# Kernel optimization log

Hardware: AMD Instinct MI355X
Metric: run time of the kernel (lower is better)

Reference implementation:

```python
import jax, jax.numpy as jnp
import numpy as np

B, T, M, F, H, O = 64, 168, 256, 32, 128, 32
TWO_OVER_PI = 2.0 / np.pi


def setup_inputs() -> dict:
    key = jax.random.key(0)
    ks = jax.random.split(key, 8)
    return {
        "x": jax.random.normal(ks[0], (B, T, M, F), dtype=jnp.float32),
        "assoc_W": jax.random.normal(ks[1], (F, M, M), dtype=jnp.float32) * (1.0 / np.sqrt(M)),
        "W_ih": jax.random.normal(ks[2], (4 * H, F), dtype=jnp.float32) * (1.0 / np.sqrt(F)),
        "W_hh": jax.random.normal(ks[3], (4 * H, H), dtype=jnp.float32) * (1.0 / np.sqrt(H)),
        "b_ih": jax.random.normal(ks[4], (4 * H,), dtype=jnp.float32) * 0.01,
        "b_hh": jax.random.normal(ks[5], (4 * H,), dtype=jnp.float32) * 0.01,
        "dense_W": jax.random.normal(ks[6], (O, H), dtype=jnp.float32) * (1.0 / np.sqrt(H)),
        "dense_b": jax.random.normal(ks[7], (O,), dtype=jnp.float32) * 0.01,
    }


def _forward(x, assoc_W, W_ih, W_hh, b_ih, b_hh, dense_W, dense_b):
    # x: [B, T, M, F] (batch_first) -> scan over time
    xt = jnp.transpose(x, (1, 0, 2, 3))  # [T, B, M, F]
    b, m = x.shape[0], x.shape[2]
    h0 = jnp.zeros((b, m, H), dtype=x.dtype)
    c0 = jnp.zeros((b, m, H), dtype=x.dtype)

    def step(carry, xin):
        h, c = carry
        # ArcTanNorm: squash into (-1, 1)
        y = jnp.arctan(xin) * TWO_OVER_PI                      # [B, M, F]
        # ICFA: per-attribute association across map units
        y = jnp.einsum('amn,bna->bma', assoc_W, y)             # [B, M, F]
        # LSTM cell (shared weights across map units), PyTorch gate order i,f,g,o
        gates = (jnp.einsum('bmf,gf->bmg', y, W_ih) + b_ih
                 + jnp.einsum('bmh,gh->bmg', h, W_hh) + b_hh)  # [B, M, 4H]
        i, f, g, o = jnp.split(gates, 4, axis=-1)
        i, f, o = jax.nn.sigmoid(i), jax.nn.sigmoid(f), jax.nn.sigmoid(o)
        g = jnp.tanh(g)
        c = f * c + i * g
        h = o * jnp.tanh(c)
        # Dense output head
        out = jnp.einsum('bmh,oh->bmo', h, dense_W) + dense_b  # [B, M, O]
        return (h, c), out

    _, outs = jax.lax.scan(step, (h0, c0), xt)                 # [T, B, M, O]
    return jnp.transpose(outs, (1, 0, 2, 3))                   # [B, T, M, O]


def reference(x, assoc_W, W_ih, W_hh, b_ih, b_hh, dense_W, dense_b):
    return _forward(x, assoc_W, W_ih, W_hh, b_ih, b_hh, dense_W, dense_b)
```

## Files before the change

### kernel.cpp

```cpp
#include <hip/hip_runtime.h>

#define B_  64
#define T_  168
#define M_  256
#define F_  32
#define H_  128
#define O_  32
#define BT_ (B_*T_)

typedef __attribute__((ext_vector_type(8))) short bh8;
typedef __attribute__((ext_vector_type(4))) short sh4;
typedef __attribute__((ext_vector_type(4))) float fx4;

static __device__ __forceinline__ short f2bf(float f) {
  unsigned u = __float_as_uint(f);
  u += 0x7FFFu + ((u >> 16) & 1u);
  return (short)(u >> 16);
}
static __device__ __forceinline__ unsigned cvtpk(float lo, float hi) {
  unsigned r;
  asm("v_cvt_pk_bf16_f32 %0, %1, %2" : "=v"(r) : "v"(lo), "v"(hi));
  return r;
}
static __device__ __forceinline__ float ex2_(float x) {
#if __has_builtin(__builtin_amdgcn_exp2f)
  return __builtin_amdgcn_exp2f(x);
#else
  return exp2f(x);
#endif
}
static __device__ __forceinline__ float rcp_(float x) {
#if __has_builtin(__builtin_amdgcn_rcpf)
  return __builtin_amdgcn_rcpf(x);
#else
  return 1.0f / x;
#endif
}
static __device__ __forceinline__ float sigm(float x) {
  return 1.0f / (1.0f + __expf(-x));
}
static __device__ __forceinline__ float tanh_f(float x) {
  return 1.0f - 2.0f / (1.0f + __expf(2.0f * x));
}
static __device__ __forceinline__ fx4 mm16(bh8 a, bh8 b, fx4 c) {
  return __builtin_amdgcn_mfma_f32_16x16x32_bf16(a, b, c, 0, 0, 0);
}
static __device__ __forceinline__ bh8 cvt8(fx4 p0, fx4 p1) {
  bh8 s;
  s[0] = f2bf(p0[0]); s[1] = f2bf(p0[1]); s[2] = f2bf(p0[2]); s[3] = f2bf(p0[3]);
  s[4] = f2bf(p1[0]); s[5] = f2bf(p1[1]); s[6] = f2bf(p1[2]); s[7] = f2bf(p1[3]);
  return s;
}


__global__ __launch_bounds__(512) void atan_tr(const float* __restrict__ x,
                                               short* __restrict__ ut) {
  __shared__ __align__(16) short tl[8 * 32 * 68];
  const int tid = threadIdx.x;
  const float c2p = 0.63661977236758134f;
  for (int it = 0; it < 21; ++it) {
    const int id = blockIdx.x + it * 256;
    const int bt0 = (id >> 2) * 8, n0 = (id & 3) * 64;
    if (it) __syncthreads();
#pragma unroll
    for (int i = 0; i < 8; ++i) {
      int idx = tid + i * 512;
      int aq = idx & 7, nl = (idx >> 3) & 63, btl = idx >> 9;
      const float* src = x + (long)(bt0 + btl) * 8192 + (n0 + nl) * 32 + aq * 4;
      fx4 v = *(const fx4*)src;
      int base = (btl * 32 + aq * 4) * 68 + nl;
#pragma unroll
      for (int k = 0; k < 4; ++k)
        tl[base + k * 68] = f2bf(atanf(v[k]) * c2p);
    }
    __syncthreads();
#pragma unroll
    for (int p = 0; p < 8; ++p) {
      int r = p * 32 + (tid >> 4);
      int a = r >> 3, btl = r & 7, nq = tid & 15;
      sh4 v = *(const sh4*)&tl[(btl * 32 + a) * 68 + nq * 4];
      *(sh4*)&ut[((long)a * BT_ + bt0 + btl) * 256 + n0 + nq * 4] = v;
    }
  }
}

__global__ __launch_bounds__(512) void icfa_gemm(const short* __restrict__ ut,
                                                 const float* __restrict__ aw,
                                                 short* __restrict__ y) {
  __shared__ __align__(16) short waf[8 * 8 * 64 * 8];
  __shared__ __align__(16) short ubf[64 * 256];
  const int tid = threadIdx.x;
  const int lane = tid & 63, w = tid >> 6, l15 = lane & 15, l4 = lane >> 4;
  const int a = blockIdx.x >> 3, s = blockIdx.x & 7;
  const long ua = (long)a * BT_;

  for (int mh = 0; mh < 2; ++mh) {
    __syncthreads();
    for (int i = 0; i < 8; ++i) {
      int idx = tid + i * 512;
      int ln = idx & 63, ks = (idx >> 6) & 7, mt = idx >> 9;
      const float* src = aw + a * 65536 + (mh * 128 + mt * 16 + (ln & 15)) * 256
                         + ks * 32 + (ln >> 4) * 8;
      *(bh8*)&waf[idx * 8] = cvt8(*(const fx4*)src, *(const fx4*)(src + 4));
    }
    __syncthreads();
    bh8 Af[8];
#pragma unroll
    for (int ks = 0; ks < 8; ++ks)
      Af[ks] = *(const bh8*)&waf[((w * 8 + ks) * 64 + lane) * 8];

    for (int tile = 0; tile < 21; ++tile) {
      const int bt0 = s * 1344 + tile * 64;
      __syncthreads();
#pragma unroll
      for (int i = 0; i < 4; ++i) {
        int idx = tid + i * 512;
        int row = idx >> 5, slot = idx & 31;
        bh8 v = *(const bh8*)&ut[(ua + bt0 + row) * 256 + slot * 8];
        int sb = (row * 512 + slot * 16) ^ ((row & 7) << 4);
        *(bh8*)&((char*)ubf)[sb] = v;
      }
      __syncthreads();
#pragma unroll
      for (int ct = 0; ct < 4; ++ct) {
        fx4 acc = {0.f, 0.f, 0.f, 0.f};
        const int btr = ct * 16 + l15;
#pragma unroll
        for (int ks = 0; ks < 8; ++ks) {
          int byo = (btr * 512 + ks * 64 + l4 * 16) ^ ((btr & 7) << 4);
          bh8 Bf = *(const bh8*)&((char*)ubf)[byo];
          acc = mm16(Af[ks], Bf, acc);
        }
        sh4 o;
        o[0] = f2bf(acc[0]); o[1] = f2bf(acc[1]);
        o[2] = f2bf(acc[2]); o[3] = f2bf(acc[3]);
        *(sh4*)&y[(ua + bt0 + btr) * 256 + mh * 128 + w * 16 + l4 * 4] = o;
      }
    }
  }
}

__global__ __launch_bounds__(1024) void lstm_fused6(
    const short* __restrict__ y,
    const float* __restrict__ Wih, const float* __restrict__ Whh,
    const float* __restrict__ bih, const float* __restrict__ bhh,
    const float* __restrict__ dW,  const float* __restrict__ db,
    float* __restrict__ out) {
  __shared__ __align__(16) short whf[65536];
  __shared__ __align__(16) short hx[8704];
  __shared__ __align__(16) short ytr[2048];
  const int tid = threadIdx.x;
  const int lane = tid & 63, w = tid >> 6, l15 = lane & 15, l4 = lane >> 4;
  const int wg = w & 7, hw = w >> 3;
  const int bidx = blockIdx.x >> 2, m0 = (blockIdx.x & 3) * 64;
  const float L2E = 1.4426950408889634f;

  for (int i = 0; i < 8; ++i) {
    int idx = tid + i * 1024;
    int ln = idx & 63, ks = (idx >> 6) & 3, gate = (idx >> 8) & 3, wgp = idx >> 10;
    const float* src = Whh + ((gate * 8 + wgp) * 16 + (ln & 15)) * 128
                       + ks * 32 + (ln >> 4) * 8;
    *(bh8*)&whf[idx * 8] = cvt8(*(const fx4*)src, *(const fx4*)(src + 4));
  }
  for (int i = 0; i < 5; ++i) {
    int j = tid + i * 1024;
    if (j < 4352) ((int*)hx)[j] = 0;
  }

  bh8 wfih[4]; float nb[4][4];
#pragma unroll
  for (int gate = 0; gate < 4; ++gate) {
    int grow = (gate * 8 + wg) * 16;
    const float* src = Wih + (grow + l15) * 32 + l4 * 8;
    wfih[gate] = cvt8(*(const fx4*)src, *(const fx4*)(src + 4));
#pragma unroll
    for (int r = 0; r < 4; ++r) {
      int g = grow + l4 * 4 + r;
      float b = bih[g] + bhh[g];
      nb[gate][r] = (gate == 2) ? (2.0f * L2E * b) : (-L2E * b);
    }
  }
  bh8 df[4]; float dbv[4];
  const int oc = wg & 1, mt_d = hw * 2 + ((wg >> 1) & 1);
#pragma unroll
  for (int ks = 0; ks < 4; ++ks) {
    const float* src = dW + (oc * 16 + l15) * 128 + ks * 32 + l4 * 8;
    df[ks] = cvt8(*(const fx4*)src, *(const fx4*)(src + 4));
  }
#pragma unroll
  for (int r = 0; r < 4; ++r) dbv[r] = db[oc * 16 + l4 * 4 + r];

  float cst[2][4];
#pragma unroll
  for (int mt = 0; mt < 2; ++mt)
#pragma unroll
    for (int r = 0; r < 4; ++r) cst[mt][r] = 0.f;

  char* hxc = (char*)hx;
  const int hrb = (hw * 32 + l15) * 272 + l4 * 16;
  const int hdb = (mt_d * 16 + l15) * 272 + l4 * 16;
  const int hwb = (hw * 32 + l15) * 272 + wg * 32 + l4 * 8;
  const int ar = tid >> 5, mq2 = tid & 31;
  const long yrow = (long)ar * BT_ + (long)bidx * T_;
  const int ml0 = mq2 * 2;
  const int R0 = (ml0 >> 4) * 64 + ((ar >> 3) << 4) + (ml0 & 15);
  const int ytre0 = R0 * 8 + (ar & 7);
  const long obB = (long)bidx * T_ * 8192
                 + (long)(m0 + mt_d * 16 + l15) * 32 + oc * 16 + l4 * 4;

  int ys = *(const int*)&y[(yrow + 0) * 256 + m0 + mq2 * 2];
  ytr[ytre0]     = (short)(ys & 0xffff);
  ytr[ytre0 + 8] = (short)(((unsigned)ys) >> 16);
  ys = *(const int*)&y[(yrow + 1) * 256 + m0 + mq2 * 2];
  __syncthreads();

  for (int t = 0; t < T_; ++t) {
    int ysn = 0;
    if (t + 2 < T_) ysn = *(const int*)&y[(yrow + t + 2) * 256 + m0 + mq2 * 2];
    fx4 acc[4][2];
    {
      bh8 yB0 = *(const bh8*)&ytr[((2 * hw) * 64 + lane) * 8];
      bh8 yB1 = *(const bh8*)&ytr[((2 * hw + 1) * 64 + lane) * 8];
      fx4 Z = {0.f, 0.f, 0.f, 0.f};
#pragma unroll
      for (int g = 0; g < 4; ++g) {
        acc[g][0] = mm16(wfih[g], yB0, Z);
        acc[g][1] = mm16(wfih[g], yB1, Z);
      }
    }
#pragma unroll
    for (int ks = 0; ks < 4; ++ks) {
      bh8 hB0 = *(const bh8*)(hxc + hrb + ks * 64);
      bh8 hB1 = *(const bh8*)(hxc + hrb + 4352 + ks * 64);
#pragma unroll
      for (int g = 0; g < 4; ++g) {
        bh8 Af = *(const bh8*)((const char*)whf
                               + ((wg * 16 + g * 4 + ks) * 64 + lane) * 16);
        acc[g][0] = mm16(Af, hB0, acc[g][0]);
        acc[g][1] = mm16(Af, hB1, acc[g][1]);
      }
    }
    if (wg < 4 && t > 0) {
      fx4 A = {dbv[0], dbv[1], dbv[2], dbv[3]};
#pragma unroll
      for (int ks = 0; ks < 4; ++ks) {
        bh8 hd = *(const bh8*)(hxc + hdb + ks * 64);
        A = mm16(df[ks], hd, A);
      }
      *(fx4*)&out[obB + (long)(t - 1) * 8192] = A;
    }
    float hn[2][4];
#pragma unroll
    for (int mt = 0; mt < 2; ++mt)
#pragma unroll
      for (int r = 0; r < 4; ++r) {
        float iv = rcp_(1.f + ex2_(fmaf(acc[0][mt][r], -L2E, nb[0][r])));
        float fv = rcp_(1.f + ex2_(fmaf(acc[1][mt][r], -L2E, nb[1][r])));
        float ov = rcp_(1.f + ex2_(fmaf(acc[3][mt][r], -L2E, nb[3][r])));
        float gv = 1.f - 2.f * rcp_(1.f + ex2_(fmaf(acc[2][mt][r], 2.f * L2E, nb[2][r])));
        float cn = fv * cst[mt][r] + iv * gv;
        cst[mt][r] = cn;
        float th = 1.f - 2.f * rcp_(1.f + ex2_(cn * (2.f * L2E)));
        hn[mt][r] = ov * th;
      }
    __syncthreads();
#pragma unroll
    for (int mt = 0; mt < 2; ++mt) {
      unsigned p01 = cvtpk(hn[mt][0], hn[mt][1]);
      unsigned p23 = cvtpk(hn[mt][2], hn[mt][3]);
      *(unsigned long long*)(hxc + hwb + mt * 4352) =
          (((unsigned long long)p23) << 32) | p01;
    }
    if (t + 1 < T_) {
      ytr[ytre0]     = (short)(ys & 0xffff);
      ytr[ytre0 + 8] = (short)(((unsigned)ys) >> 16);
    }
    ys = ysn;
    __syncthreads();
  }
  if (wg < 4) {
    fx4 A = {dbv[0], dbv[1], dbv[2], dbv[3]};
#pragma unroll
    for (int ks = 0; ks < 4; ++ks) {
      bh8 hd = *(const bh8*)(hxc + hdb + ks * 64);
      A = mm16(df[ks], hd, A);
    }
    *(fx4*)&out[obB + (long)(T_ - 1) * 8192] = A;
  }
}


__global__ __launch_bounds__(512) void icfa_mfma(const float* __restrict__ x,
                                                 const float* __restrict__ aw,
                                                 float* __restrict__ y) {
  __shared__ short waf[8 * 8 * 64 * 8];
  __shared__ short ubf[64 * 264];
  const int tid = threadIdx.x;
  const int lane = tid & 63, w = tid >> 6, l15 = lane & 15, l4 = lane >> 4;
  const int a = blockIdx.x >> 3, s = blockIdx.x & 7;
  const float c2p = 0.63661977236758134f;

  for (int mh = 0; mh < 2; ++mh) {
    __syncthreads();
    for (int i = 0; i < 8; ++i) {
      int idx = tid + i * 512;
      int ln = idx & 63, ks = (idx >> 6) & 7, mt = idx >> 9;
      const float* src = aw + a * 65536 + (mh * 128 + mt * 16 + (ln & 15)) * 256
                         + ks * 32 + (ln >> 4) * 8;
      *(bh8*)&waf[idx * 8] = cvt8(*(const fx4*)src, *(const fx4*)(src + 4));
    }
    __syncthreads();
    bh8 Af[8];
#pragma unroll
    for (int ks = 0; ks < 8; ++ks)
      Af[ks] = *(const bh8*)&waf[((w * 8 + ks) * 64 + lane) * 8];

    for (int tile = 0; tile < 21; ++tile) {
      const int bt0 = s * 1344 + tile * 64;
      __syncthreads();
#pragma unroll 4
      for (int i = 0; i < 32; ++i) {
        int idx = tid + i * 512;
        int n = idx & 255, btc = idx >> 8;
        float v = x[(long)(bt0 + btc) * 8192 + n * 32 + a];
        ubf[btc * 264 + n] = f2bf(atanf(v) * c2p);
      }
      __syncthreads();
#pragma unroll
      for (int ct = 0; ct < 4; ++ct) {
        fx4 acc = {0.f, 0.f, 0.f, 0.f};
#pragma unroll
        for (int ks = 0; ks < 8; ++ks) {
          bh8 Bf = *(const bh8*)&ubf[(ct * 16 + l15) * 264 + ks * 32 + l4 * 8];
          acc = mm16(Af[ks], Bf, acc);
        }
        long ybase = (long)(bt0 + ct * 16 + l15) * 8192
                     + (mh * 128 + w * 16 + l4 * 4) * 32 + a;
#pragma unroll
        for (int r = 0; r < 4; ++r) y[ybase + (long)r * 32] = acc[r];
      }
    }
  }
}

__global__ __launch_bounds__(512) void lstm_fused(
    const float* __restrict__ Wih, const float* __restrict__ Whh,
    const float* __restrict__ bih, const float* __restrict__ bhh,
    const float* __restrict__ dW,  const float* __restrict__ db,
    float* __restrict__ yo) {
  __shared__ short whf[32 * 4 * 64 * 8];
  __shared__ short hbuf[4 * 4 * 64 * 8];
  __shared__ short ytr[4 * 64 * 8];
  __shared__ float obuf[64 * 36];
  const int tid = threadIdx.x;
  const int lane = tid & 63, w = tid >> 6, l15 = lane & 15, l4 = lane >> 4;
  const int bidx = blockIdx.x >> 2, m0 = (blockIdx.x & 3) * 64;

  for (int i = 0; i < 16; ++i) {
    int idx = tid + i * 512;
    int ln = idx & 63, ks = (idx >> 6) & 3, ct = idx >> 8;
    const float* src = Whh + (ct * 16 + (ln & 15)) * 128 + ks * 32 + (ln >> 4) * 8;
    *(bh8*)&whf[idx * 8] = cvt8(*(const fx4*)src, *(const fx4*)(src + 4));
  }
  for (int i = 0; i < 8; ++i) ((int*)hbuf)[tid + i * 512] = 0;

  bh8 wfih[4]; float bias[4];
#pragma unroll
  for (int gate = 0; gate < 4; ++gate) {
    int g = (gate * 8 + w) * 16 + l15;
    bias[gate] = bih[g] + bhh[g];
    const float* src = Wih + g * 32 + l4 * 8;
    wfih[gate] = cvt8(*(const fx4*)src, *(const fx4*)(src + 4));
  }
  bh8 df[4];
  const int rtd = w >> 1, oc = w & 1;
  const int od = oc * 16 + l15;
  const float dbias = db[od];
#pragma unroll
  for (int ks = 0; ks < 4; ++ks) {
    const float* src = dW + od * 128 + ks * 32 + l4 * 8;
    df[ks] = cvt8(*(const fx4*)src, *(const fx4*)(src + 4));
  }

  float cst[4][4];
#pragma unroll
  for (int rt = 0; rt < 4; ++rt)
#pragma unroll
    for (int r = 0; r < 4; ++r) cst[rt][r] = 0.f;

  const int mloc = tid >> 3, a0 = (tid & 7) * 4;
  const long tb0 = (long)bidx * T_ * 8192;
  const long pfoff = (long)(m0 + mloc) * 32 + a0;
  const int ytre = ((mloc >> 4) * 64 + ((a0 >> 3) << 4) + (mloc & 15)) * 8 + (a0 & 7);
  const int kse = w >> 1;
  const int lnhi = (((w & 1) * 2 + (l15 >> 3)) << 4);
  const int e0 = l15 & 7;

  fx4 y4 = *(const fx4*)&yo[tb0 + pfoff];
  {
    sh4 p; p[0] = f2bf(y4[0]); p[1] = f2bf(y4[1]); p[2] = f2bf(y4[2]); p[3] = f2bf(y4[3]);
    *(sh4*)&ytr[ytre] = p;
  }
  y4 = *(const fx4*)&yo[tb0 + 8192 + pfoff];
  __syncthreads();

  for (int t = 0; t < T_; ++t) {
    const long off = tb0 + (long)t * 8192;
    float hn[4][4];
    bh8 Ball[4][4];
#pragma unroll
    for (int gate = 0; gate < 4; ++gate)
#pragma unroll
      for (int ks = 0; ks < 4; ++ks)
        Ball[gate][ks] =
            *(const bh8*)&whf[((((gate * 8 + w) * 4) + ks) * 64 + lane) * 8];
#pragma unroll
    for (int rt = 0; rt < 4; ++rt) {
      bh8 ya = *(const bh8*)&ytr[(rt * 64 + lane) * 8];
      bh8 hA[4];
#pragma unroll
      for (int ks = 0; ks < 4; ++ks)
        hA[ks] = *(const bh8*)&hbuf[((rt * 4 + ks) * 64 + lane) * 8];
      fx4 acc[4];
#pragma unroll
      for (int gate = 0; gate < 4; ++gate) {
        fx4 A = {bias[gate], bias[gate], bias[gate], bias[gate]};
        A = mm16(ya, wfih[gate], A);
#pragma unroll
        for (int ks = 0; ks < 4; ++ks) A = mm16(hA[ks], Ball[gate][ks], A);
        acc[gate] = A;
      }
#pragma unroll
      for (int r = 0; r < 4; ++r) {
        float iv = sigm(acc[0][r]);
        float fv = sigm(acc[1][r]);
        float gv = tanh_f(acc[2][r]);
        float ov = sigm(acc[3][r]);
        float cn = fv * cst[rt][r] + iv * gv;
        cst[rt][r] = cn;
        hn[rt][r] = ov * tanh_f(cn);
      }
    }
    __syncthreads();
#pragma unroll
    for (int rt = 0; rt < 4; ++rt)
#pragma unroll
      for (int r = 0; r < 4; ++r)
        hbuf[((rt * 4 + kse) * 64 + lnhi + l4 * 4 + r) * 8 + e0] = f2bf(hn[rt][r]);
    if (t + 1 < T_) {
      sh4 p; p[0] = f2bf(y4[0]); p[1] = f2bf(y4[1]); p[2] = f2bf(y4[2]); p[3] = f2bf(y4[3]);
      *(sh4*)&ytr[ytre] = p;
    }
    if (t + 2 < T_) y4 = *(const fx4*)&yo[off + 2 * 8192 + pfoff];
    __syncthreads();
    {
      fx4 A = {dbias, dbias, dbias, dbias};
#pragma unroll
      for (int ks = 0; ks < 4; ++ks) {
        bh8 hA2 = *(const bh8*)&hbuf[((rtd * 4 + ks) * 64 + lane) * 8];
        A = mm16(hA2, df[ks], A);
      }
#pragma unroll
      for (int r = 0; r < 4; ++r)
        obuf[(rtd * 16 + l4 * 4 + r) * 36 + oc * 16 + l15] = A[r];
    }
    __syncthreads();
    {
      fx4 o4 = *(const fx4*)&obuf[mloc * 36 + a0];
      *(fx4*)&yo[off + pfoff] = o4;
    }
  }
}

extern "C" void kernel_launch(void* const* d_in, const int* in_sizes, int n_in,
                              void* d_out, int out_size, void* d_ws, size_t ws_size,
                              hipStream_t stream) {
  const float* x   = (const float*)d_in[0];
  const float* aw  = (const float*)d_in[1];
  const float* wih = (const float*)d_in[2];
  const float* whh = (const float*)d_in[3];
  const float* bih = (const float*)d_in[4];
  const float* bhh = (const float*)d_in[5];
  const float* dw  = (const float*)d_in[6];
  const float* db  = (const float*)d_in[7];
  float* out = (float*)d_out;

  const size_t PLANE = (size_t)32 * BT_ * 256;
  const size_t NEED  = 2 * PLANE * sizeof(short);
  if (d_ws && ws_size >= NEED) {
    short* u = (short*)d_ws;
    short* yv = u + PLANE;
    hipLaunchKernelGGL(atan_tr,   dim3(256), dim3(512), 0, stream, x, u);
    hipLaunchKernelGGL(icfa_gemm, dim3(256), dim3(512), 0, stream, u, aw, yv);
    hipLaunchKernelGGL(lstm_fused6, dim3(256), dim3(1024), 0, stream,
                       yv, wih, whh, bih, bhh, dw, db, out);
  } else {
    hipLaunchKernelGGL(icfa_mfma, dim3(256), dim3(512), 0, stream, x, aw, out);
    hipLaunchKernelGGL(lstm_fused, dim3(256), dim3(512), 0, stream,
                       wih, whh, bih, bhh, dw, db, out);
  }
}
```

Baseline: 854.6 us.

## Double-buffer LSTM h/y LDS tiles, keep input-gate weights in registers, fuse gate math

Double-buffers the hidden-state and input tiles in shared memory, so each timestep needs one barrier instead of two; new h is written to the alternate buffer. The input-gate W_hh fragment now lives in registers, which frees LDS and cuts per-step LDS reads. The sigmoid/tanh gate math is rewritten algebraically to share reciprocals, giving fewer rcp instructions. Costs are more registers and LDS for the doubled buffers, plus a possible small numerical change from the combined reciprocals.

```diff
diff --git a/kernel.cpp b/kernel.cpp
--- a/kernel.cpp
+++ b/kernel.cpp
@@ -140,31 +140,37 @@
   }
 }
 
-__global__ __launch_bounds__(1024) void lstm_fused6(
+__global__ __launch_bounds__(1024) void lstm_fused7(
     const short* __restrict__ y,
     const float* __restrict__ Wih, const float* __restrict__ Whh,
     const float* __restrict__ bih, const float* __restrict__ bhh,
     const float* __restrict__ dW,  const float* __restrict__ db,
     float* __restrict__ out) {
-  __shared__ __align__(16) short whf[65536];
-  __shared__ __align__(16) short hx[8704];
-  __shared__ __align__(16) short ytr[2048];
+  __shared__ __align__(16) short whf[49152];
+  __shared__ __align__(16) short hx[17408];
+  __shared__ __align__(16) short ytr[4096];
   const int tid = threadIdx.x;
   const int lane = tid & 63, w = tid >> 6, l15 = lane & 15, l4 = lane >> 4;
   const int wg = w & 7, hw = w >> 3;
   const int bidx = blockIdx.x >> 2, m0 = (blockIdx.x & 3) * 64;
   const float L2E = 1.4426950408889634f;
 
-  for (int i = 0; i < 8; ++i) {
+  for (int i = 0; i < 6; ++i) {
     int idx = tid + i * 1024;
-    int ln = idx & 63, ks = (idx >> 6) & 3, gate = (idx >> 8) & 3, wgp = idx >> 10;
-    const float* src = Whh + ((gate * 8 + wgp) * 16 + (ln & 15)) * 128
+    int ln = idx & 63, ks = (idx >> 6) & 3, wgp = (idx >> 8) & 7, gm1 = idx >> 11;
+    const float* src = Whh + (((gm1 + 1) * 8 + wgp) * 16 + (ln & 15)) * 128
                        + ks * 32 + (ln >> 4) * 8;
     *(bh8*)&whf[idx * 8] = cvt8(*(const fx4*)src, *(const fx4*)(src + 4));
   }
-  for (int i = 0; i < 5; ++i) {
+  for (int i = 0; i < 9; ++i) {
     int j = tid + i * 1024;
-    if (j < 4352) ((int*)hx)[j] = 0;
+    if (j < 8704) ((int*)hx)[j] = 0;
+  }
+  bh8 wrg[4];
+#pragma unroll
+  for (int ks = 0; ks < 4; ++ks) {
+    const float* src = Whh + (wg * 16 + l15) * 128 + ks * 32 + l4 * 8;
+    wrg[ks] = cvt8(*(const fx4*)src, *(const fx4*)(src + 4));
   }
 
   bh8 wfih[4]; float nb[4][4];
@@ -214,13 +220,14 @@
   ys = *(const int*)&y[(yrow + 1) * 256 + m0 + mq2 * 2];
   __syncthreads();
 
+  int pbo = 0, pbi = 0;
   for (int t = 0; t < T_; ++t) {
     int ysn = 0;
     if (t + 2 < T_) ysn = *(const int*)&y[(yrow + t + 2) * 256 + m0 + mq2 * 2];
     fx4 acc[4][2];
     {
-      bh8 yB0 = *(const bh8*)&ytr[((2 * hw) * 64 + lane) * 8];
-      bh8 yB1 = *(const bh8*)&ytr[((2 * hw + 1) * 64 + lane) * 8];
+      bh8 yB0 = *(const bh8*)&ytr[pbi + ((2 * hw) * 64 + lane) * 8];
+      bh8 yB1 = *(const bh8*)&ytr[pbi + ((2 * hw + 1) * 64 + lane) * 8];
       fx4 Z = {0.f, 0.f, 0.f, 0.f};
 #pragma unroll
       for (int g = 0; g < 4; ++g) {
@@ -230,12 +237,14 @@
     }
 #pragma unroll
     for (int ks = 0; ks < 4; ++ks) {
-      bh8 hB0 = *(const bh8*)(hxc + hrb + ks * 64);
-      bh8 hB1 = *(const bh8*)(hxc + hrb + 4352 + ks * 64);
-#pragma unroll
-      for (int g = 0; g < 4; ++g) {
+      bh8 hB0 = *(const bh8*)(hxc + pbo + hrb + ks * 64);
+      bh8 hB1 = *(const bh8*)(hxc + pbo + hrb + 4352 + ks * 64);
+      acc[0][0] = mm16(wrg[ks], hB0, acc[0][0]);
+      acc[0][1] = mm16(wrg[ks], hB1, acc[0][1]);
+#pragma unroll
+      for (int g = 1; g < 4; ++g) {
         bh8 Af = *(const bh8*)((const char*)whf
-                               + ((wg * 16 + g * 4 + ks) * 64 + lane) * 16);
+                               + (g - 1) * 32768 + wg * 4096 + ks * 1024 + lane * 16);
         acc[g][0] = mm16(Af, hB0, acc[g][0]);
         acc[g][1] = mm16(Af, hB1, acc[g][1]);
       }
@@ -244,7 +253,7 @@
       fx4 A = {dbv[0], dbv[1], dbv[2], dbv[3]};
 #pragma unroll
       for (int ks = 0; ks < 4; ++ks) {
-        bh8 hd = *(const bh8*)(hxc + hdb + ks * 64);
+        bh8 hd = *(const bh8*)(hxc + pbo + hdb + ks * 64);
         A = mm16(df[ks], hd, A);
       }
       *(fx4*)&out[obB + (long)(t - 1) * 8192] = A;
@@ -254,35 +263,38 @@
     for (int mt = 0; mt < 2; ++mt)
 #pragma unroll
       for (int r = 0; r < 4; ++r) {
-        float iv = rcp_(1.f + ex2_(fmaf(acc[0][mt][r], -L2E, nb[0][r])));
-        float fv = rcp_(1.f + ex2_(fmaf(acc[1][mt][r], -L2E, nb[1][r])));
-        float ov = rcp_(1.f + ex2_(fmaf(acc[3][mt][r], -L2E, nb[3][r])));
-        float gv = 1.f - 2.f * rcp_(1.f + ex2_(fmaf(acc[2][mt][r], 2.f * L2E, nb[2][r])));
-        float cn = fv * cst[mt][r] + iv * gv;
+        float eI = ex2_(fmaf(acc[0][mt][r], -L2E, nb[0][r]));
+        float eF = ex2_(fmaf(acc[1][mt][r], -L2E, nb[1][r]));
+        float eG = ex2_(fmaf(acc[2][mt][r], 2.f * L2E, nb[2][r]));
+        float eO = ex2_(fmaf(acc[3][mt][r], -L2E, nb[3][r]));
+        float pi = 1.f + eI, pf = 1.f + eF, pg = 1.f + eG;
+        float pig = pi * pg;
+        float num = fmaf(cst[mt][r], pig, (eG - 1.f) * pf);
+        float cn = num * rcp_(pf * pig);
         cst[mt][r] = cn;
-        float th = 1.f - 2.f * rcp_(1.f + ex2_(cn * (2.f * L2E)));
-        hn[mt][r] = ov * th;
-      }
-    __syncthreads();
+        float eC = ex2_(cn * (2.f * L2E));
+        hn[mt][r] = (eC - 1.f) * rcp_((1.f + eO) * (1.f + eC));
+      }
 #pragma unroll
     for (int mt = 0; mt < 2; ++mt) {
       unsigned p01 = cvtpk(hn[mt][0], hn[mt][1]);
       unsigned p23 = cvtpk(hn[mt][2], hn[mt][3]);
-      *(unsigned long long*)(hxc + hwb + mt * 4352) =
+      *(unsigned long long*)(hxc + (pbo ^ 17408) + hwb + mt * 4352) =
           (((unsigned long long)p23) << 32) | p01;
     }
     if (t + 1 < T_) {
-      ytr[ytre0]     = (short)(ys & 0xffff);
-      ytr[ytre0 + 8] = (short)(((unsigned)ys) >> 16);
+      ytr[(pbi ^ 2048) + ytre0]     = (short)(ys & 0xffff);
+      ytr[(pbi ^ 2048) + ytre0 + 8] = (short)(((unsigned)ys) >> 16);
     }
     ys = ysn;
     __syncthreads();
+    pbo ^= 17408; pbi ^= 2048;
   }
   if (wg < 4) {
     fx4 A = {dbv[0], dbv[1], dbv[2], dbv[3]};
 #pragma unroll
     for (int ks = 0; ks < 4; ++ks) {
-      bh8 hd = *(const bh8*)(hxc + hdb + ks * 64);
+      bh8 hd = *(const bh8*)(hxc + pbo + hdb + ks * 64);
       A = mm16(df[ks], hd, A);
     }
     *(fx4*)&out[obB + (long)(T_ - 1) * 8192] = A;
@@ -492,7 +504,7 @@
     short* yv = u + PLANE;
     hipLaunchKernelGGL(atan_tr,   dim3(256), dim3(512), 0, stream, x, u);
     hipLaunchKernelGGL(icfa_gemm, dim3(256), dim3(512), 0, stream, u, aw, yv);
-    hipLaunchKernelGGL(lstm_fused6, dim3(256), dim3(1024), 0, stream,
+    hipLaunchKernelGGL(lstm_fused7, dim3(256), dim3(1024), 0, stream,
                        yv, wih, whh, bih, bhh, dw, db, out);
   } else {
     hipLaunchKernelGGL(icfa_mfma, dim3(256), dim3(512), 0, stream, x, aw, out);
```

Result: slower. 933.3 us (+9.2%).

## Keep recurrent LSTM weights in registers and halve block size

Applied to the files above, without the earlier changes.

The LSTM kernel drops the 128KB shared-memory copy of W_hh and keeps each wave's W_hh fragments in registers. Blocks shrink from 1024 to 512 threads, with each wave covering all four 16-row m-tiles instead of two. The aim is to remove per-step LDS weight reads and the large LDS footprint, and to allow two blocks per CU under the new launch bounds. In exchange, register pressure rises (64 extra VGPRs of weights plus doubled accumulators and cell state), which risks spilling or lower occupancy. Fewer waves are also available to hide the serial per-timestep latency.

```diff
diff --git a/kernel.cpp b/kernel.cpp
--- a/kernel.cpp
+++ b/kernel.cpp
@@ -140,32 +140,31 @@
   }
 }
 
-__global__ __launch_bounds__(1024) void lstm_fused6(
+__global__ __launch_bounds__(512, 2) void lstm_fused8(
     const short* __restrict__ y,
     const float* __restrict__ Wih, const float* __restrict__ Whh,
     const float* __restrict__ bih, const float* __restrict__ bhh,
     const float* __restrict__ dW,  const float* __restrict__ db,
     float* __restrict__ out) {
-  __shared__ __align__(16) short whf[65536];
   __shared__ __align__(16) short hx[8704];
   __shared__ __align__(16) short ytr[2048];
   const int tid = threadIdx.x;
-  const int lane = tid & 63, w = tid >> 6, l15 = lane & 15, l4 = lane >> 4;
-  const int wg = w & 7, hw = w >> 3;
+  const int lane = tid & 63, wg = tid >> 6, l15 = lane & 15, l4 = lane >> 4;
   const int bidx = blockIdx.x >> 2, m0 = (blockIdx.x & 3) * 64;
   const float L2E = 1.4426950408889634f;
 
-  for (int i = 0; i < 8; ++i) {
-    int idx = tid + i * 1024;
-    int ln = idx & 63, ks = (idx >> 6) & 3, gate = (idx >> 8) & 3, wgp = idx >> 10;
-    const float* src = Whh + ((gate * 8 + wgp) * 16 + (ln & 15)) * 128
-                       + ks * 32 + (ln >> 4) * 8;
-    *(bh8*)&whf[idx * 8] = cvt8(*(const fx4*)src, *(const fx4*)(src + 4));
-  }
-  for (int i = 0; i < 5; ++i) {
-    int j = tid + i * 1024;
+  for (int i = 0; i < 9; ++i) {
+    int j = tid + i * 512;
     if (j < 4352) ((int*)hx)[j] = 0;
   }
+  bh8 wrg[4][4];
+#pragma unroll
+  for (int g = 0; g < 4; ++g)
+#pragma unroll
+    for (int ks = 0; ks < 4; ++ks) {
+      const float* src = Whh + ((g * 8 + wg) * 16 + l15) * 128 + ks * 32 + l4 * 8;
+      wrg[g][ks] = cvt8(*(const fx4*)src, *(const fx4*)(src + 4));
+    }
 
   bh8 wfih[4]; float nb[4][4];
 #pragma unroll
@@ -181,7 +180,7 @@
     }
   }
   bh8 df[4]; float dbv[4];
-  const int oc = wg & 1, mt_d = hw * 2 + ((wg >> 1) & 1);
+  const int oc = wg >> 2, mt_d = wg & 3;
 #pragma unroll
   for (int ks = 0; ks < 4; ++ks) {
     const float* src = dW + (oc * 16 + l15) * 128 + ks * 32 + l4 * 8;
@@ -190,57 +189,57 @@
 #pragma unroll
   for (int r = 0; r < 4; ++r) dbv[r] = db[oc * 16 + l4 * 4 + r];
 
-  float cst[2][4];
-#pragma unroll
-  for (int mt = 0; mt < 2; ++mt)
+  float cst[4][4];
+#pragma unroll
+  for (int mt = 0; mt < 4; ++mt)
 #pragma unroll
     for (int r = 0; r < 4; ++r) cst[mt][r] = 0.f;
 
   char* hxc = (char*)hx;
-  const int hrb = (hw * 32 + l15) * 272 + l4 * 16;
+  const int hrb = l15 * 272 + l4 * 16;
   const int hdb = (mt_d * 16 + l15) * 272 + l4 * 16;
-  const int hwb = (hw * 32 + l15) * 272 + wg * 32 + l4 * 8;
-  const int ar = tid >> 5, mq2 = tid & 31;
+  const int hwb = l15 * 272 + wg * 32 + l4 * 8;
+  const int ar = tid >> 4, mq = tid & 15;
   const long yrow = (long)ar * BT_ + (long)bidx * T_;
-  const int ml0 = mq2 * 2;
-  const int R0 = (ml0 >> 4) * 64 + ((ar >> 3) << 4) + (ml0 & 15);
-  const int ytre0 = R0 * 8 + (ar & 7);
+  const int ytre = ((mq >> 2) * 64 + ((ar >> 3) << 4) + (mq & 3) * 4) * 8 + (ar & 7);
   const long obB = (long)bidx * T_ * 8192
                  + (long)(m0 + mt_d * 16 + l15) * 32 + oc * 16 + l4 * 4;
 
-  int ys = *(const int*)&y[(yrow + 0) * 256 + m0 + mq2 * 2];
-  ytr[ytre0]     = (short)(ys & 0xffff);
-  ytr[ytre0 + 8] = (short)(((unsigned)ys) >> 16);
-  ys = *(const int*)&y[(yrow + 1) * 256 + m0 + mq2 * 2];
+  sh4 ys = *(const sh4*)&y[(yrow + 0) * 256 + m0 + mq * 4];
+#pragma unroll
+  for (int j = 0; j < 4; ++j) ytr[ytre + j * 8] = ys[j];
+  ys = *(const sh4*)&y[(yrow + 1) * 256 + m0 + mq * 4];
   __syncthreads();
 
   for (int t = 0; t < T_; ++t) {
-    int ysn = 0;
-    if (t + 2 < T_) ysn = *(const int*)&y[(yrow + t + 2) * 256 + m0 + mq2 * 2];
-    fx4 acc[4][2];
+    sh4 ysn = {0, 0, 0, 0};
+    if (t + 2 < T_) ysn = *(const sh4*)&y[(yrow + t + 2) * 256 + m0 + mq * 4];
+    fx4 acc[4][4];
     {
-      bh8 yB0 = *(const bh8*)&ytr[((2 * hw) * 64 + lane) * 8];
-      bh8 yB1 = *(const bh8*)&ytr[((2 * hw + 1) * 64 + lane) * 8];
+      bh8 yB[4];
+#pragma unroll
+      for (int mt = 0; mt < 4; ++mt)
+        yB[mt] = *(const bh8*)&ytr[(mt * 64 + lane) * 8];
       fx4 Z = {0.f, 0.f, 0.f, 0.f};
 #pragma unroll
-      for (int g = 0; g < 4; ++g) {
-        acc[g][0] = mm16(wfih[g], yB0, Z);
-        acc[g][1] = mm16(wfih[g], yB1, Z);
-      }
+      for (int g = 0; g < 4; ++g)
+#pragma unroll
+        for (int mt = 0; mt < 4; ++mt)
+          acc[g][mt] = mm16(wfih[g], yB[mt], Z);
     }
 #pragma unroll
     for (int ks = 0; ks < 4; ++ks) {
-      bh8 hB0 = *(const bh8*)(hxc + hrb + ks * 64);
-      bh8 hB1 = *(const bh8*)(hxc + hrb + 4352 + ks * 64);
-#pragma unroll
-      for (int g = 0; g < 4; ++g) {
-        bh8 Af = *(const bh8*)((const char*)whf
-                               + ((wg * 16 + g * 4 + ks) * 64 + lane) * 16);
-        acc[g][0] = mm16(Af, hB0, acc[g][0]);
-        acc[g][1] = mm16(Af, hB1, acc[g][1]);
-      }
-    }
-    if (wg < 4 && t > 0) {
+      bh8 hB[4];
+#pragma unroll
+      for (int mt = 0; mt < 4; ++mt)
+        hB[mt] = *(const bh8*)(hxc + hrb + mt * 4352 + ks * 64);
+#pragma unroll
+      for (int g = 0; g < 4; ++g)
+#pragma unroll
+        for (int mt = 0; mt < 4; ++mt)
+          acc[g][mt] = mm16(wrg[g][ks], hB[mt], acc[g][mt]);
+    }
+    if (t > 0) {
       fx4 A = {dbv[0], dbv[1], dbv[2], dbv[3]};
 #pragma unroll
       for (int ks = 0; ks < 4; ++ks) {
@@ -249,9 +248,9 @@
       }
       *(fx4*)&out[obB + (long)(t - 1) * 8192] = A;
     }
-    float hn[2][4];
-#pragma unroll
-    for (int mt = 0; mt < 2; ++mt)
+    float hn[4][4];
+#pragma unroll
+    for (int mt = 0; mt < 4; ++mt)
 #pragma unroll
       for (int r = 0; r < 4; ++r) {
         float iv = rcp_(1.f + ex2_(fmaf(acc[0][mt][r], -L2E, nb[0][r])));
@@ -265,20 +264,20 @@
       }
     __syncthreads();
 #pragma unroll
-    for (int mt = 0; mt < 2; ++mt) {
+    for (int mt = 0; mt < 4; ++mt) {
       unsigned p01 = cvtpk(hn[mt][0], hn[mt][1]);
       unsigned p23 = cvtpk(hn[mt][2], hn[mt][3]);
       *(unsigned long long*)(hxc + hwb + mt * 4352) =
           (((unsigned long long)p23) << 32) | p01;
     }
     if (t + 1 < T_) {
-      ytr[ytre0]     = (short)(ys & 0xffff);
-      ytr[ytre0 + 8] = (short)(((unsigned)ys) >> 16);
+#pragma unroll
+      for (int j = 0; j < 4; ++j) ytr[ytre + j * 8] = ys[j];
     }
     ys = ysn;
     __syncthreads();
   }
-  if (wg < 4) {
+  {
     fx4 A = {dbv[0], dbv[1], dbv[2], dbv[3]};
 #pragma unroll
     for (int ks = 0; ks < 4; ++ks) {
@@ -492,7 +491,7 @@
     short* yv = u + PLANE;
     hipLaunchKernelGGL(atan_tr,   dim3(256), dim3(512), 0, stream, x, u);
     hipLaunchKernelGGL(icfa_gemm, dim3(256), dim3(512), 0, stream, u, aw, yv);
-    hipLaunchKernelGGL(lstm_fused6, dim3(256), dim3(1024), 0, stream,
+    hipLaunchKernelGGL(lstm_fused8, dim3(256), dim3(512), 0, stream,
                        yv, wih, whh, bih, bhh, dw, db, out);
   } else {
     hipLaunchKernelGGL(icfa_mfma, dim3(256), dim3(512), 0, stream, x, aw, out);
```

New measurement: 886.3 us. 1.04x slower.
